# Kernel optimization log

Hardware: AMD Instinct MI355X
Metric: run time of the kernel (lower is better)

## Reference

```python
import jax, jax.numpy as jnp
import numpy as np


def setup_inputs() -> dict:
    key = jax.random.key(0)
    k1, k2, k3, k4 = jax.random.split(key, 4)
    B, I, P, F = 4096, 1024, 512, 2048
    x = jax.random.normal(k1, (B, I), dtype=jnp.float32)
    # params initialized like torch.rand(...)*2-1 (uniform in [-1,1])
    features = jax.random.uniform(k2, (F, I), dtype=jnp.float32, minval=-1.0, maxval=1.0)
    prototypes = jax.random.uniform(k3, (P, I), dtype=jnp.float32, minval=-1.0, maxval=1.0)
    # scalars: torch inits to zeros; use small nonzero values so output/grads are informative
    abt = jax.random.normal(k4, (3,), dtype=jnp.float32) * 0.1
    alpha = abt[0:1]
    beta = abt[1:2]
    theta = abt[2:3]
    return {"x": x, "features": features, "prototypes": prototypes,
            "alpha": alpha, "beta": beta, "theta": theta}


def reference(x, features, prototypes, alpha, beta, theta):
    # x: [b, i], features: [f, i], prototypes: [p, i]
    # Original einsums broadcast over p but the projection is p-independent:
    xf = x @ features.T            # [b, f]
    pf = prototypes @ features.T   # [p, f]
    x_pres = jax.nn.relu(xf)       # [b, f]
    p_pres = jax.nn.relu(pf)       # [p, f]
    # common[b,p]       = sum_f xf*pf*relu(xf)*relu(pf)
    # x_distinct[b,p]   = sum_f xf*relu(xf)*(1-relu(pf))
    # p_distinct[b,p]   = sum_f pf*relu(pf)*(1-relu(xf))
    a = xf * x_pres                # [b, f]
    c = pf * p_pres                # [p, f]
    common = a @ c.T                                   # [b, p]
    x_distinctive = a @ (1.0 - p_pres).T               # [b, p]
    p_distinctive = (1.0 - x_pres) @ c.T               # [b, p]
    return theta * common - alpha * x_distinctive - beta * p_distinctive
```

## Files before the change

kernel.cpp:

```cpp
#include <hip/hip_runtime.h>
#include <cstdint>

typedef __attribute__((ext_vector_type(8))) short bf16x8;
typedef __attribute__((ext_vector_type(16))) float f32x16;
typedef __attribute__((ext_vector_type(4))) float f4;
typedef __attribute__((ext_vector_type(8))) unsigned short u16x8;
typedef unsigned short u16;


__device__ __forceinline__ u16 f2bf(float f) {
  uint32_t u = __builtin_bit_cast(uint32_t, f);
  u += 0x7fffu + ((u >> 16) & 1u);
  return (u16)(u >> 16);
}

__device__ __forceinline__ float bf2f(u16 h) {
  return __builtin_bit_cast(float, (uint32_t)h << 16);
}

__device__ __forceinline__ void async_cp16(const void* g, void* l) {
  __builtin_amdgcn_global_load_lds(
      (const __attribute__((address_space(1))) uint32_t*)g,
      (__attribute__((address_space(3))) uint32_t*)l, 16, 0, 0);
}

__global__ __launch_bounds__(256) void cast3(
    const float* __restrict__ x, const float* __restrict__ f,
    const float* __restrict__ p, u16* __restrict__ dst,
    int n1, int n2, int n3) {
  int i = (blockIdx.x * 256 + threadIdx.x) * 8;
  const float* src;
  int local;
  if (i < n1) { src = x; local = i; }
  else if (i < n1 + n2) { src = f; local = i - n1; }
  else if (i < n1 + n2 + n3) { src = p; local = i - n1 - n2; }
  else return;
  f4 a = *(const f4*)(src + local);
  f4 b = *(const f4*)(src + local + 4);
  u16x8 o;
  o[0] = f2bf(a.x); o[1] = f2bf(a.y); o[2] = f2bf(a.z); o[3] = f2bf(a.w);
  o[4] = f2bf(b.x); o[5] = f2bf(b.y); o[6] = f2bf(b.z); o[7] = f2bf(b.w);
  *(u16x8*)(dst + i) = o;
}


__device__ __forceinline__ void stage_tile(
    const u16* __restrict__ A, const u16* __restrict__ B, int K,
    int k0, int tid, u16* L) {
  constexpr int TM = 128, TN = 128;
  const int wave = tid >> 6;
  #pragma unroll
  for (int it = 0; it < TM / 32; ++it) {
    int c = it * 256 + tid;
    int row = c >> 3, pc = c & 7;
    int gc = pc ^ (row & 7);
    async_cp16(A + (size_t)row * K + (k0 + gc * 8),
               &L[(it * 256 + wave * 64) * 8]);
  }
  #pragma unroll
  for (int it = 0; it < TN / 32; ++it) {
    int c = it * 256 + tid;
    int row = c >> 3, pc = c & 7;
    int gc = pc ^ (row & 7);
    async_cp16(B + (size_t)row * K + (k0 + gc * 8),
               &L[TM * 64 + (it * 256 + wave * 64) * 8]);
  }
}

__device__ __forceinline__ void compute_tile(
    const u16* L, int lane, int wrow, int wcol, f32x16 (&acc)[2][2]) {
  constexpr int TM = 128;
  #pragma unroll
  for (int s = 0; s < 4; ++s) {
    const int h = s * 2 + (lane >> 5);
    bf16x8 bfr[2], afr[2];
    #pragma unroll
    for (int j = 0; j < 2; ++j) {
      const int rb = wcol * 64 + j * 32 + (lane & 31);
      bfr[j] = *(const bf16x8*)&L[TM * 64 + (rb * 8 + (h ^ (rb & 7))) * 8];
    }
    #pragma unroll
    for (int i = 0; i < 2; ++i) {
      const int ra = wrow * 64 + i * 32 + (lane & 31);
      afr[i] = *(const bf16x8*)&L[(ra * 8 + (h ^ (ra & 7))) * 8];
    }
    #pragma unroll
    for (int i = 0; i < 2; ++i)
      #pragma unroll
      for (int j = 0; j < 2; ++j)
        acc[i][j] = __builtin_amdgcn_mfma_f32_32x32x16_bf16(
            afr[i], bfr[j], acc[i][j], 0, 0, 0);
  }
}

__device__ __forceinline__ void mainloop(
    const u16* __restrict__ A, const u16* __restrict__ B, int K,
    int kbeg, int kend, int tid, u16* lds, f32x16 (&acc)[2][2]) {
  constexpr int BK = 64;
  constexpr int BUF = 16384;
  const int lane = tid & 63;
  const int wave = tid >> 6;
  const int wrow = wave >> 1, wcol = wave & 1;

  stage_tile(A, B, K, kbeg, tid, lds);
  int cur = 0;
  for (int k0 = kbeg; k0 < kend; k0 += BK) {
    if (k0 + BK < kend) {
      stage_tile(A, B, K, k0 + BK, tid, lds + (cur ^ 1) * BUF);
      asm volatile("s_waitcnt vmcnt(8)" ::: "memory");
    } else {
      asm volatile("s_waitcnt vmcnt(0)" ::: "memory");
    }
    __builtin_amdgcn_s_barrier();
    compute_tile(lds + cur * BUF, lane, wrow, wcol, acc);
    __builtin_amdgcn_s_barrier();
    cur ^= 1;
  }
}


__global__ __launch_bounds__(256) void gemm12(
    const u16* __restrict__ xb, const u16* __restrict__ pb,
    const u16* __restrict__ fb, u16* __restrict__ Acat, u16* __restrict__ Bcat,
    const float* __restrict__ alpha, const float* __restrict__ beta,
    const float* __restrict__ theta) {
  constexpr int TM = 128, K = 1024, N = 2048;
  constexpr int TSTRIDE = 136;
  __shared__ u16 lds[32768];

  const int tid = threadIdx.x;
  const int lane = tid & 63;
  const int wave = tid >> 6;
  const int wrow = wave >> 1, wcol = wave & 1;

  const int bid = blockIdx.x;
  const int xcd = bid & 7, slot = bid >> 3;
  const int xt = (xcd & 3) * 9 + (slot >> 3);
  const int yt = (xcd >> 2) * 8 + (slot & 7);

  const int bm_all = xt * TM;
  const int bn = yt * 128;
  const bool is_x = bm_all < 4096;
  const u16* A = is_x ? xb + (size_t)bm_all * K : pb + (size_t)(bm_all - 4096) * K;
  const u16* B = fb + (size_t)bn * K;

  f32x16 acc[2][2] = {};
  mainloop(A, B, K, 0, K, tid, lds, acc);

  float th = 0.f, al = 0.f, be = 0.f;
  if (!is_x) { th = theta[0]; al = alpha[0]; be = beta[0]; }
  u16* dst = is_x ? Acat : Bcat;
  const int rowbase = is_x ? bm_all : bm_all - 4096;
  const int rquad = 4 * (lane >> 5);

  #pragma unroll
  for (int half = 0; half < 2; ++half) {
    __syncthreads();
    #pragma unroll
    for (int i = 0; i < 2; ++i) {
      #pragma unroll
      for (int j = 0; j < 2; ++j) {
        const int cl = wcol * 64 + j * 32 + (lane & 31);
        #pragma unroll
        for (int r = 0; r < 16; ++r) {
          const int rl = wrow * 64 + i * 32 + (r & 3) + 8 * (r >> 2) + rquad;
          float v = acc[i][j][r];
          float pres = v > 0.f ? v : 0.f;
          float o;
          if (is_x) o = half == 0 ? v * pres : 1.f - pres;
          else {
            float cc = v * pres;
            o = half == 0 ? th * cc - al * (1.f - pres) : -be * cc;
          }
          lds[rl * TSTRIDE + cl] = f2bf(o);
        }
      }
    }
    __syncthreads();
    #pragma unroll
    for (int v = 0; v < 8; ++v) {
      const int rl = v * 16 + (tid >> 4);
      const int c8 = (tid & 15) * 8;
      u16x8 vec = *(const u16x8*)&lds[rl * TSTRIDE + c8];
      *(u16x8*)&dst[(size_t)(rowbase + rl) * (2 * N) + bn + c8 + half * N] = vec;
    }
  }
}

__global__ __launch_bounds__(256) void gemm3(
    const u16* __restrict__ Acat, const u16* __restrict__ Bcat,
    u16* __restrict__ part) {
  constexpr int TM = 128, TN = 128, K = 4096, KSPLIT = 4;
  __shared__ u16 lds[32768];

  const int tid = threadIdx.x;

  const int bid = blockIdx.x;
  const int xcd = bid & 7, slot = bid >> 3;
  const int bz = xcd >> 1;
  const int bxt = (xcd & 1) * 16 + (slot >> 2);
  const int byt = slot & 3;

  const int bm = bxt * TM;
  const int bn = byt * TN;
  const int kbeg = bz * (K / KSPLIT);
  const int kend = kbeg + (K / KSPLIT);

  f32x16 acc[2][2] = {};
  mainloop(Acat + (size_t)bm * K, Bcat + (size_t)bn * K, K, kbeg, kend,
           tid, lds, acc);

  const size_t pbase = ((size_t)bz * 128 + byt * 32 + bxt) * 16384;
  #pragma unroll
  for (int i = 0; i < 2; ++i)
    #pragma unroll
    for (int j = 0; j < 2; ++j)
      #pragma unroll
      for (int h = 0; h < 2; ++h) {
        u16x8 o;
        #pragma unroll
        for (int e = 0; e < 8; ++e) o[e] = f2bf(acc[i][j][h * 8 + e]);
        *(u16x8*)&part[pbase + (size_t)(i * 4 + j * 2 + h) * 2048 + tid * 8] = o;
      }
}

__global__ __launch_bounds__(256) void reduce4(
    const u16* __restrict__ part, float* __restrict__ out) {
  constexpr int N = 512;
  const int tid = threadIdx.x;
  const int lane = tid & 63;
  const int wave = tid >> 6;
  const int wrow = wave >> 1, wcol = wave & 1;
  const int tileId = blockIdx.x >> 3;
  const int q = blockIdx.x & 7;
  const int bm = (tileId & 31) * 128;
  const int bn = (tileId >> 5) * 128;

  float v[8] = {};
  #pragma unroll
  for (int z = 0; z < 4; ++z) {
    u16x8 u = *(const u16x8*)&part[((size_t)z * 128 + tileId) * 16384 +
                                   (size_t)q * 2048 + tid * 8];
    #pragma unroll
    for (int e = 0; e < 8; ++e) v[e] += bf2f(u[e]);
  }
  const int i = q >> 2, j = (q >> 1) & 1, h = q & 1;
  const int gc = bn + wcol * 64 + j * 32 + (lane & 31);
  const int grb = bm + wrow * 64 + i * 32 + 4 * (lane >> 5);
  #pragma unroll
  for (int e = 0; e < 8; ++e) {
    const int reg = h * 8 + e;
    out[(size_t)(grb + (reg & 3) + 8 * (reg >> 2)) * N + gc] = v[e];
  }
}

extern "C" void kernel_launch(void* const* d_in, const int* in_sizes, int n_in,
                              void* d_out, int out_size, void* d_ws, size_t ws_size,
                              hipStream_t stream) {
  const float* x     = (const float*)d_in[0];
  const float* feat  = (const float*)d_in[1];
  const float* proto = (const float*)d_in[2];
  const float* alpha = (const float*)d_in[3];
  const float* beta  = (const float*)d_in[4];
  const float* theta = (const float*)d_in[5];
  float* out = (float*)d_out;

  constexpr int Bb = 4096, Ii = 1024, Pp = 512, Ff = 2048;

  char* ws = (char*)d_ws;
  u16* xb   = (u16*)ws;
  u16* fb   = xb + (size_t)Bb * Ii;
  u16* pb   = fb + (size_t)Ff * Ii;
  size_t r0 = 33554432;
  u16* Acat = (u16*)(ws + r0);
  u16* Bcat = Acat + (size_t)Bb * 2 * Ff;
  u16* part = Bcat + (size_t)Pp * 2 * Ff;

  const int n1 = Bb * Ii, n2 = Ff * Ii, n3 = Pp * Ii;
  cast3<<<((n1 + n2 + n3) / 8 + 255) / 256, 256, 0, stream>>>(
      x, feat, proto, xb, n1, n2, n3);

  gemm12<<<576, 256, 0, stream>>>(xb, pb, fb, Acat, Bcat, alpha, beta, theta);

  gemm3<<<512, 256, 0, stream>>>(Acat, Bcat, part);

  reduce4<<<1024, 256, 0, stream>>>(part, out);
}
```

Measured before the change: 138.0 us.

## Use 512-thread blocks with 8 waves per 128x128 tile in all GEMM kernels

```diff
diff --git a/kernel.cpp b/kernel.cpp
--- a/kernel.cpp
+++ b/kernel.cpp
@@ -44,82 +44,71 @@
 }
 
 
-__device__ __forceinline__ void stage_tile(
+__device__ __forceinline__ void stage_tile512(
     const u16* __restrict__ A, const u16* __restrict__ B, int K,
     int k0, int tid, u16* L) {
-  constexpr int TM = 128, TN = 128;
-  const int wave = tid >> 6;
-  #pragma unroll
-  for (int it = 0; it < TM / 32; ++it) {
-    int c = it * 256 + tid;
+  const int wave = tid >> 6;
+  #pragma unroll
+  for (int it = 0; it < 2; ++it) {
+    int c = it * 512 + tid;
     int row = c >> 3, pc = c & 7;
     int gc = pc ^ (row & 7);
     async_cp16(A + (size_t)row * K + (k0 + gc * 8),
-               &L[(it * 256 + wave * 64) * 8]);
-  }
-  #pragma unroll
-  for (int it = 0; it < TN / 32; ++it) {
-    int c = it * 256 + tid;
+               &L[(it * 512 + wave * 64) * 8]);
+  }
+  #pragma unroll
+  for (int it = 0; it < 2; ++it) {
+    int c = it * 512 + tid;
     int row = c >> 3, pc = c & 7;
     int gc = pc ^ (row & 7);
     async_cp16(B + (size_t)row * K + (k0 + gc * 8),
-               &L[TM * 64 + (it * 256 + wave * 64) * 8]);
-  }
-}
-
-__device__ __forceinline__ void compute_tile(
-    const u16* L, int lane, int wrow, int wcol, f32x16 (&acc)[2][2]) {
-  constexpr int TM = 128;
+               &L[8192 + (it * 512 + wave * 64) * 8]);
+  }
+}
+
+__device__ __forceinline__ void compute_tile512(
+    const u16* L, int lane, int wrow, int wcol, f32x16 (&acc)[2]) {
   #pragma unroll
   for (int s = 0; s < 4; ++s) {
     const int h = s * 2 + (lane >> 5);
-    bf16x8 bfr[2], afr[2];
+    const int ra = wrow * 32 + (lane & 31);
+    bf16x8 afr = *(const bf16x8*)&L[(ra * 8 + (h ^ (ra & 7))) * 8];
     #pragma unroll
     for (int j = 0; j < 2; ++j) {
       const int rb = wcol * 64 + j * 32 + (lane & 31);
-      bfr[j] = *(const bf16x8*)&L[TM * 64 + (rb * 8 + (h ^ (rb & 7))) * 8];
-    }
-    #pragma unroll
-    for (int i = 0; i < 2; ++i) {
-      const int ra = wrow * 64 + i * 32 + (lane & 31);
-      afr[i] = *(const bf16x8*)&L[(ra * 8 + (h ^ (ra & 7))) * 8];
-    }
-    #pragma unroll
-    for (int i = 0; i < 2; ++i)
-      #pragma unroll
-      for (int j = 0; j < 2; ++j)
-        acc[i][j] = __builtin_amdgcn_mfma_f32_32x32x16_bf16(
-            afr[i], bfr[j], acc[i][j], 0, 0, 0);
-  }
-}
-
-__device__ __forceinline__ void mainloop(
+      bf16x8 bfr = *(const bf16x8*)&L[8192 + (rb * 8 + (h ^ (rb & 7))) * 8];
+      acc[j] = __builtin_amdgcn_mfma_f32_32x32x16_bf16(afr, bfr, acc[j], 0, 0, 0);
+    }
+  }
+}
+
+__device__ __forceinline__ void mainloop512(
     const u16* __restrict__ A, const u16* __restrict__ B, int K,
-    int kbeg, int kend, int tid, u16* lds, f32x16 (&acc)[2][2]) {
+    int kbeg, int kend, int tid, u16* lds, f32x16 (&acc)[2]) {
   constexpr int BK = 64;
   constexpr int BUF = 16384;
   const int lane = tid & 63;
   const int wave = tid >> 6;
   const int wrow = wave >> 1, wcol = wave & 1;
 
-  stage_tile(A, B, K, kbeg, tid, lds);
+  stage_tile512(A, B, K, kbeg, tid, lds);
   int cur = 0;
   for (int k0 = kbeg; k0 < kend; k0 += BK) {
     if (k0 + BK < kend) {
-      stage_tile(A, B, K, k0 + BK, tid, lds + (cur ^ 1) * BUF);
-      asm volatile("s_waitcnt vmcnt(8)" ::: "memory");
+      stage_tile512(A, B, K, k0 + BK, tid, lds + (cur ^ 1) * BUF);
+      asm volatile("s_waitcnt vmcnt(4)" ::: "memory");
     } else {
       asm volatile("s_waitcnt vmcnt(0)" ::: "memory");
     }
     __builtin_amdgcn_s_barrier();
-    compute_tile(lds + cur * BUF, lane, wrow, wcol, acc);
+    compute_tile512(lds + cur * BUF, lane, wrow, wcol, acc);
     __builtin_amdgcn_s_barrier();
     cur ^= 1;
   }
 }
 
 
-__global__ __launch_bounds__(256) void gemm12(
+__global__ __launch_bounds__(512) void gemm12(
     const u16* __restrict__ xb, const u16* __restrict__ pb,
     const u16* __restrict__ fb, u16* __restrict__ Acat, u16* __restrict__ Bcat,
     const float* __restrict__ alpha, const float* __restrict__ beta,
@@ -144,8 +133,8 @@
   const u16* A = is_x ? xb + (size_t)bm_all * K : pb + (size_t)(bm_all - 4096) * K;
   const u16* B = fb + (size_t)bn * K;
 
-  f32x16 acc[2][2] = {};
-  mainloop(A, B, K, 0, K, tid, lds, acc);
+  f32x16 acc[2] = {};
+  mainloop512(A, B, K, 0, K, tid, lds, acc);
 
   float th = 0.f, al = 0.f, be = 0.f;
   if (!is_x) { th = theta[0]; al = alpha[0]; be = beta[0]; }
@@ -157,29 +146,26 @@
   for (int half = 0; half < 2; ++half) {
     __syncthreads();
     #pragma unroll
-    for (int i = 0; i < 2; ++i) {
+    for (int j = 0; j < 2; ++j) {
+      const int cl = wcol * 64 + j * 32 + (lane & 31);
       #pragma unroll
-      for (int j = 0; j < 2; ++j) {
-        const int cl = wcol * 64 + j * 32 + (lane & 31);
-        #pragma unroll
-        for (int r = 0; r < 16; ++r) {
-          const int rl = wrow * 64 + i * 32 + (r & 3) + 8 * (r >> 2) + rquad;
-          float v = acc[i][j][r];
-          float pres = v > 0.f ? v : 0.f;
-          float o;
-          if (is_x) o = half == 0 ? v * pres : 1.f - pres;
-          else {
-            float cc = v * pres;
-            o = half == 0 ? th * cc - al * (1.f - pres) : -be * cc;
-          }
-          lds[rl * TSTRIDE + cl] = f2bf(o);
+      for (int r = 0; r < 16; ++r) {
+        const int rl = wrow * 32 + (r & 3) + 8 * (r >> 2) + rquad;
+        float v = acc[j][r];
+        float pres = v > 0.f ? v : 0.f;
+        float o;
+        if (is_x) o = half == 0 ? v * pres : 1.f - pres;
+        else {
+          float cc = v * pres;
+          o = half == 0 ? th * cc - al * (1.f - pres) : -be * cc;
         }
+        lds[rl * TSTRIDE + cl] = f2bf(o);
       }
     }
     __syncthreads();
     #pragma unroll
-    for (int v = 0; v < 8; ++v) {
-      const int rl = v * 16 + (tid >> 4);
+    for (int v = 0; v < 4; ++v) {
+      const int rl = v * 32 + (tid >> 4);
       const int c8 = (tid & 15) * 8;
       u16x8 vec = *(const u16x8*)&lds[rl * TSTRIDE + c8];
       *(u16x8*)&dst[(size_t)(rowbase + rl) * (2 * N) + bn + c8 + half * N] = vec;
@@ -187,7 +173,7 @@
   }
 }
 
-__global__ __launch_bounds__(256) void gemm3(
+__global__ __launch_bounds__(512) void gemm3(
     const u16* __restrict__ Acat, const u16* __restrict__ Bcat,
     u16* __restrict__ part) {
   constexpr int TM = 128, TN = 128, K = 4096, KSPLIT = 4;
@@ -206,33 +192,31 @@
   const int kbeg = bz * (K / KSPLIT);
   const int kend = kbeg + (K / KSPLIT);
 
-  f32x16 acc[2][2] = {};
-  mainloop(Acat + (size_t)bm * K, Bcat + (size_t)bn * K, K, kbeg, kend,
-           tid, lds, acc);
+  f32x16 acc[2] = {};
+  mainloop512(Acat + (size_t)bm * K, Bcat + (size_t)bn * K, K, kbeg, kend,
+              tid, lds, acc);
 
   const size_t pbase = ((size_t)bz * 128 + byt * 32 + bxt) * 16384;
   #pragma unroll
-  for (int i = 0; i < 2; ++i)
-    #pragma unroll
-    for (int j = 0; j < 2; ++j)
+  for (int j = 0; j < 2; ++j)
+    #pragma unroll
+    for (int h = 0; h < 2; ++h) {
+      u16x8 o;
       #pragma unroll
-      for (int h = 0; h < 2; ++h) {
-        u16x8 o;
-        #pragma unroll
-        for (int e = 0; e < 8; ++e) o[e] = f2bf(acc[i][j][h * 8 + e]);
-        *(u16x8*)&part[pbase + (size_t)(i * 4 + j * 2 + h) * 2048 + tid * 8] = o;
-      }
-}
-
-__global__ __launch_bounds__(256) void reduce4(
+      for (int e = 0; e < 8; ++e) o[e] = f2bf(acc[j][h * 8 + e]);
+      *(u16x8*)&part[pbase + (size_t)(j * 2 + h) * 4096 + tid * 8] = o;
+    }
+}
+
+__global__ __launch_bounds__(512) void reduce4(
     const u16* __restrict__ part, float* __restrict__ out) {
   constexpr int N = 512;
   const int tid = threadIdx.x;
   const int lane = tid & 63;
   const int wave = tid >> 6;
   const int wrow = wave >> 1, wcol = wave & 1;
-  const int tileId = blockIdx.x >> 3;
-  const int q = blockIdx.x & 7;
+  const int tileId = blockIdx.x >> 2;
+  const int q = blockIdx.x & 3;
   const int bm = (tileId & 31) * 128;
   const int bn = (tileId >> 5) * 128;
 
@@ -240,13 +224,13 @@
   #pragma unroll
   for (int z = 0; z < 4; ++z) {
     u16x8 u = *(const u16x8*)&part[((size_t)z * 128 + tileId) * 16384 +
-                                   (size_t)q * 2048 + tid * 8];
+                                   (size_t)q * 4096 + tid * 8];
     #pragma unroll
     for (int e = 0; e < 8; ++e) v[e] += bf2f(u[e]);
   }
-  const int i = q >> 2, j = (q >> 1) & 1, h = q & 1;
+  const int j = q >> 1, h = q & 1;
   const int gc = bn + wcol * 64 + j * 32 + (lane & 31);
-  const int grb = bm + wrow * 64 + i * 32 + 4 * (lane >> 5);
+  const int grb = bm + wrow * 32 + 4 * (lane >> 5);
   #pragma unroll
   for (int e = 0; e < 8; ++e) {
     const int reg = h * 8 + e;
@@ -280,9 +264,9 @@
   cast3<<<((n1 + n2 + n3) / 8 + 255) / 256, 256, 0, stream>>>(
       x, feat, proto, xb, n1, n2, n3);
 
-  gemm12<<<576, 256, 0, stream>>>(xb, pb, fb, Acat, Bcat, alpha, beta, theta);
-
-  gemm3<<<512, 256, 0, stream>>>(Acat, Bcat, part);
-
-  reduce4<<<1024, 256, 0, stream>>>(part, out);
-}
+  gemm12<<<576, 512, 0, stream>>>(xb, pb, fb, Acat, Bcat, alpha, beta, theta);
+
+  gemm3<<<512, 512, 0, stream>>>(Acat, Bcat, part);
+
+  reduce4<<<512, 512, 0, stream>>>(part, out);
+}
```

Result: faster. 134.9 us (median of 3 runs) (-2.2%).
